# Optimization experiments

Hardware: AMD Instinct MI355X
Metric: run time of the kernel (lower is better)

## Reference

```python
import jax, jax.numpy as jnp
import numpy as np

B, F, T = 4, 2048, 2048
CF, CT = 1024, 1024
H, DH = 16, 64
ALPHA = 1.0 / np.sqrt(DH).astype(np.float32)


def setup_inputs() -> dict:
    key = jax.random.key(0)
    ks = jax.random.split(key, 8)
    s = 0.02  # trunc_normal-ish init scale
    return {
        "from_tensor": jax.random.normal(ks[0], (B, F, CF), jnp.float32),
        "to_tensor": jax.random.normal(ks[1], (B, T, CT), jnp.float32),
        "mask": jax.random.randint(ks[2], (B, F, T), 0, 2, jnp.int32),
        "Wq": jax.random.normal(ks[3], (CF, H * DH), jnp.float32) * s,
        "bq": jnp.zeros((H * DH,), jnp.float32),
        "Wk": jax.random.normal(ks[4], (CT, H * DH), jnp.float32) * s,
        "bk": jnp.zeros((H * DH,), jnp.float32),
        "Wv": jax.random.normal(ks[5], (CT, H * DH), jnp.float32) * s,
        "bv": jnp.zeros((H * DH,), jnp.float32),
    }


def reference(from_tensor, to_tensor, mask, Wq, bq, Wk, bk, Wv, bv):
    # projections (nn.Linear with no activation)
    q = from_tensor @ Wq + bq          # [B,F,H*DH]
    k = to_tensor @ Wk + bk            # [B,T,H*DH]
    v = to_tensor @ Wv + bv            # [B,T,H*DH]
    q = q.reshape(B, F, H, DH)         # query: [..., F, H, DH]
    k = k.reshape(B, T, DH, H)         # key:   [..., T, DH, H]  (self._shape[::-1])
    v = v.reshape(B, T, H, DH)
    # score = transpose(q,-3,-2) @ transpose(k,-3,-1) * alpha -> [B,H,F,T]
    score = jnp.einsum("bfhd,btdh->bhft", q, k) * ALPHA
    if mask is not None:
        adder = (1.0 - mask[:, None].astype(score.dtype)) * -100000.0  # [B,1,F,T]
        score = score + adder
    probs = jax.nn.softmax(score, axis=-1)  # dropout p=0.0 -> identity
    # context = probs @ transpose(v,-3,-2), then transpose back: [B,F,H,DH]
    context = jnp.einsum("bhft,bthd->bfhd", probs, v)
    return context.reshape(B, F, H * DH)
```

## Files before the change

kernel.cpp:

```cpp
#include <hip/hip_runtime.h>
#include <type_traits>

typedef __bf16 bf16_t;
typedef __attribute__((ext_vector_type(8))) __bf16 bf16x8;
typedef __attribute__((ext_vector_type(4))) float f32x4;
typedef __attribute__((ext_vector_type(16))) float f32x16;

__device__ __forceinline__ void async16(const void* g, void* lds) {
  __builtin_amdgcn_global_load_lds((const __attribute__((address_space(1))) unsigned int*)g,
                                   (__attribute__((address_space(3))) unsigned int*)lds, 16, 0, 0);
}

__device__ __forceinline__ unsigned pk2(float lo, float hi) {
  unsigned short a = __builtin_bit_cast(unsigned short, (__bf16)lo);
  unsigned short b = __builtin_bit_cast(unsigned short, (__bf16)hi);
  return (unsigned)a | ((unsigned)b << 16);
}

__device__ __forceinline__ void plswap(unsigned& a, unsigned& b) {
#if __has_builtin(__builtin_amdgcn_permlane32_swap)
  auto r = __builtin_amdgcn_permlane32_swap((int)a, (int)b, false, false);
  a = (unsigned)r[0];
  b = (unsigned)r[1];
#else
  const bool hb = (threadIdx.x & 32) != 0;
  unsigned bx = (unsigned)__shfl_xor((int)b, 32);
  unsigned ax = (unsigned)__shfl_xor((int)a, 32);
  unsigned na = hb ? bx : a;
  unsigned nb = hb ? b : ax;
  a = na; b = nb;
#endif
}

__global__ __launch_bounds__(256) void prep_kernel(const int* __restrict__ mask, unsigned long long* __restrict__ mb,
                                                   const float* __restrict__ Wq, const float* __restrict__ Wk,
                                                   const float* __restrict__ Wv, bf16_t* __restrict__ Wt,
                                                   const float* __restrict__ from, bf16_t* __restrict__ inbF,
                                                   const float* __restrict__ to_, bf16_t* __restrict__ inbT) {
  const int bid = blockIdx.x, tid = threadIdx.x;
  if (bid < 2048) {
    const int lane = tid & 63, w = tid >> 6;
    for (int i = 0; i < 32; ++i) {
      size_t word = (size_t)bid * 128 + (size_t)i * 4 + w;
      unsigned long long bits = __ballot(mask[word * 64 + lane] != 0);
      if (lane == 0) mb[word] = bits;
    }
  } else if (bid < 3584) {
    const int idx = bid - 2048;
    const int z = idx >> 9, r = idx & 511;
    const float* src = (z == 0) ? Wq : ((z == 1) ? Wk : Wv);
    const float sc = (z == 0) ? 0.18033688011112042f : 1.0f;
    bf16_t* dst = Wt + (size_t)z * 1024 * 1024;
    const int n = (r & 15) * 64 + (tid & 63);
    const int k8 = (r >> 4) * 4 + (tid >> 6);
    bf16x8 o;
#pragma unroll
    for (int j = 0; j < 8; ++j) o[j] = (__bf16)(src[(size_t)(k8 * 8 + j) * 1024 + n] * sc);
    *(bf16x8*)(dst + (size_t)n * 1024 + k8 * 8) = o;
  } else {
    const bool isF = bid < 7680;
    const size_t i = (size_t)(bid - (isF ? 3584 : 7680)) * 256 + tid;
    const float4* in4 = (const float4*)(isF ? from : to_);
    bf16_t* outp = isF ? inbF : inbT;
    float4 a = in4[i * 2], b = in4[i * 2 + 1];
    bf16x8 o;
    o[0] = (__bf16)a.x; o[1] = (__bf16)a.y; o[2] = (__bf16)a.z; o[3] = (__bf16)a.w;
    o[4] = (__bf16)b.x; o[5] = (__bf16)b.y; o[6] = (__bf16)b.z; o[7] = (__bf16)b.w;
    *(bf16x8*)(outp + i * 8) = o;
  }
}

__global__ __launch_bounds__(256) void proj_kernel(const bf16_t* __restrict__ inbF, const bf16_t* __restrict__ inbT,
                                                   const bf16_t* __restrict__ Wt,
                                                   const float* __restrict__ bq, const float* __restrict__ bk,
                                                   const float* __restrict__ bv,
                                                   bf16_t* __restrict__ Qw, bf16_t* __restrict__ Kw,
                                                   bf16_t* __restrict__ Vw) {
  __shared__ __align__(16) unsigned char smem[33792];
  bf16_t* se = (bf16_t*)smem;
  const int z = blockIdx.z;
  const bf16_t* A = (z == 0) ? inbF : inbT;
  const bf16_t* Wz = Wt + (size_t)z * 1024 * 1024;
  const float* bias = (z == 0) ? bq : ((z == 1) ? bk : bv);
  bf16_t* dst = (z == 0) ? Qw : ((z == 1) ? Kw : Vw);
  const float bscale = (z == 0) ? 0.18033688011112042f : 1.0f;

  const int tid = threadIdx.x, lane = tid & 63, w = tid >> 6;
  const int m0 = blockIdx.x * 128, n0 = blockIdx.y * 128;
  const int wm = (w >> 1) * 64, wn = (w & 1) * 64;
  const int r = lane & 15, kq = lane >> 4;
  const int srow = lane >> 2, sslot = lane & 3;
  f32x4 acc[4][4] = {};

  auto stage = [&](int buf, int k0) {
    bf16_t* Ad = se + buf * 4096;
    bf16_t* Bd = se + 8192 + buf * 4096;
#pragma unroll
    for (int it = 0; it < 2; ++it) {
      const int c = it * 4 + w;
      const int row = c * 16 + srow;
      async16(A + (size_t)(m0 + row) * 1024 + k0 + ((sslot ^ (row & 3)) * 8), Ad + c * 512);
      async16(Wz + (size_t)(n0 + row) * 1024 + k0 + ((sslot ^ (row & 3)) * 8), Bd + c * 512);
    }
  };

  stage(0, 0);
  __syncthreads();
  for (int tile = 0; tile < 32; ++tile) {
    const int cur = tile & 1;
    if (tile < 31) stage(cur ^ 1, (tile + 1) * 32);
    const bf16_t* Al = se + cur * 4096;
    const bf16_t* Bl = se + 8192 + cur * 4096;
    bf16x8 af[4], bfr[4];
#pragma unroll
    for (int i = 0; i < 4; ++i) {
      const int ra = wm + i * 16 + r;
      af[i] = *(const bf16x8*)(Al + ra * 32 + ((kq ^ (ra & 3)) * 8));
      const int rb = wn + i * 16 + r;
      bfr[i] = *(const bf16x8*)(Bl + rb * 32 + ((kq ^ (rb & 3)) * 8));
    }
    __builtin_amdgcn_s_setprio(1);
#pragma unroll
    for (int i = 0; i < 4; ++i)
#pragma unroll
      for (int j = 0; j < 4; ++j)
        acc[i][j] = __builtin_amdgcn_mfma_f32_16x16x32_bf16(af[i], bfr[j], acc[i][j], 0, 0, 0);
    __builtin_amdgcn_s_setprio(0);
    __syncthreads();
  }

  bf16_t* Cl = se;
  float bvv[4];
#pragma unroll
  for (int j = 0; j < 4; ++j) bvv[j] = bias[n0 + wn + j * 16 + r] * bscale;
#pragma unroll
  for (int i = 0; i < 4; ++i)
#pragma unroll
    for (int j = 0; j < 4; ++j)
#pragma unroll
      for (int g = 0; g < 4; ++g)
        Cl[(wm + i * 16 + kq * 4 + g) * 132 + wn + j * 16 + r] = (__bf16)(acc[i][j][g] + bvv[j]);
  __syncthreads();

  const int b = m0 >> 11, sbase = m0 & 2047;
  if (z == 0) {
#pragma unroll
    for (int q = 0; q < 8; ++q) {
      const int cid = q * 256 + tid;
      const int m = cid >> 4, c = (cid >> 3) & 1, d8 = cid & 7;
      bf16x8 val = *(const bf16x8*)(Cl + m * 132 + c * 64 + d8 * 8);
      *(bf16x8*)(dst + ((size_t)(b * 16 + (n0 >> 6) + c) * 2048 + sbase + m) * 64 + d8 * 8) = val;
    }
  } else if (z == 1) {
#pragma unroll
    for (int q = 0; q < 8; ++q) {
      const int cid = q * 256 + tid;
      const int hh = cid >> 7, m = cid & 127;
      bf16x8 val;
#pragma unroll
      for (int dd = 0; dd < 8; ++dd) val[dd] = Cl[m * 132 + dd * 16 + hh];
      *(bf16x8*)(dst + ((size_t)(b * 16 + hh) * 2048 + sbase + m) * 64 + (n0 >> 4)) = val;
    }
  } else {
#pragma unroll
    for (int q = 0; q < 8; ++q) {
      const int cid = q * 256 + tid;
      const int nl = cid >> 4, m8 = cid & 15;
      bf16x8 val;
#pragma unroll
      for (int s = 0; s < 8; ++s) val[s] = Cl[(m8 * 8 + s) * 132 + nl];
      const int hh = (n0 >> 6) + (nl >> 6), dd = nl & 63;
      *(bf16x8*)(dst + ((size_t)(b * 16 + hh) * 64 + dd) * 2048 + sbase + m8 * 8) = val;
    }
  }
}

__global__ __launch_bounds__(256, 2) void attn_kernel(const bf16_t* __restrict__ Q, const bf16_t* __restrict__ K,
                                                      const bf16_t* __restrict__ VT,
                                                      const unsigned long long* __restrict__ mb,
                                                      float* __restrict__ out) {
  __shared__ __align__(16) unsigned char smem[65536];
  bf16_t* se = (bf16_t*)smem;
  const int tid = threadIdx.x, lane = tid & 63, w = tid >> 6;
  const int cl = lane & 31, hi = lane >> 5;

  const int lid = blockIdx.x + 8 * (blockIdx.y + 16 * blockIdx.z);
  const int xcd = lid & 7, q_ = lid >> 3;
  const int pairIdx = xcd * 8 + (q_ & 7);
  const int f0 = (q_ >> 3) * 256;
  const int h = pairIdx & 15, b = pairIdx >> 4;

  const size_t bh = (size_t)b * 16 + h;
  const int fw = f0 + w * 64;

  const bf16_t* Qb = Q + (bh * 2048 + fw) * 64;
  bf16x8 qf[2][4];
#pragma unroll
  for (int fb = 0; fb < 2; ++fb)
#pragma unroll
    for (int ks = 0; ks < 4; ++ks)
      qf[fb][ks] = *(const bf16x8*)(Qb + (fb * 32 + cl) * 64 + ks * 16 + hi * 8);

  f32x16 Of[2][2] = {};
  float lacc[2] = {0.f, 0.f};
  bf16x8 paw[2][4];

  const unsigned long long* mrow[2];
  mrow[0] = mb + ((size_t)b * 2048 + fw + cl) * 32;
  mrow[1] = mb + ((size_t)b * 2048 + fw + 32 + cl) * 32;

  const int row8 = lane >> 3, slot = lane & 7;
  const int swz = (slot ^ row8) * 8;
  const bf16_t* kgb[2];
  const bf16_t* vgb[2];
#pragma unroll
  for (int it = 0; it < 2; ++it) {
    const int row = it * 32 + w * 8 + row8;
    kgb[it] = K + (bh * 2048 + row) * 64 + swz;
    vgb[it] = VT + (bh * 64 + row) * 2048 + swz;
  }

  auto stage_k = [&](int buf, int tile) {
    bf16_t* kd = se + buf * 4096 + w * 512;
#pragma unroll
    for (int it = 0; it < 2; ++it)
      async16(kgb[it] + (size_t)tile * 4096, kd + it * 2048);
  };
  auto stage_v = [&](int buf, int tile) {
    bf16_t* vd = se + 16384 + buf * 4096 + w * 512;
#pragma unroll
    for (int it = 0; it < 2; ++it)
      async16(vgb[it] + (size_t)tile * 64, vd + it * 2048);
  };

  auto pv_step = [&](int vs) {
    const bf16_t* Vl = se + 16384 + vs * 4096;
    __builtin_amdgcn_s_setprio(1);
#pragma unroll
    for (int db = 0; db < 2; ++db) {
      const int vrow0 = db * 32 + cl;
#pragma unroll
      for (int kt = 0; kt < 4; ++kt) {
        bf16x8 vf = *(const bf16x8*)(Vl + vrow0 * 64 + (((2 * kt + hi) ^ (vrow0 & 7)) * 8));
        Of[0][db] = __builtin_amdgcn_mfma_f32_32x32x16_bf16(paw[0][kt], vf, Of[0][db], 0, 0, 0);
        Of[1][db] = __builtin_amdgcn_mfma_f32_32x32x16_bf16(paw[1][kt], vf, Of[1][db], 0, 0, 0);
      }
    }
    __builtin_amdgcn_s_setprio(0);
  };

  unsigned long long m[4][2];
  stage_k(0, 0); stage_v(0, 0);
  stage_k(1, 1); stage_v(1, 1);
  m[0][0] = mrow[0][0];
  m[0][1] = mrow[1][0];

  auto body = [&](auto Sc, auto lastc, int tile) {
    constexpr int S = decltype(Sc)::value;
    constexpr bool last = decltype(lastc)::value;
    if constexpr (last) {
      asm volatile("s_waitcnt vmcnt(0)" ::: "memory");
    } else {
      asm volatile("s_waitcnt vmcnt(6)" ::: "memory");
    }
    __builtin_amdgcn_s_barrier();
    __builtin_amdgcn_sched_barrier(0);
    if (tile + 2 < 32) {
      stage_k((S + 2) & 3, tile + 2);
      stage_v((S + 2) & 3, tile + 2);
    }
    if (tile + 1 < 32) {
      m[(S + 1) & 3][0] = mrow[0][tile + 1];
      m[(S + 1) & 3][1] = mrow[1][tile + 1];
    }
    const bf16_t* Kl = se + S * 4096;

    f32x16 st0[2], st1[2];
#pragma unroll
    for (int fb = 0; fb < 2; ++fb) {
      const unsigned nm0 = ~((unsigned)(m[S][fb] >> (4 * hi)));
      const unsigned nm1 = ~((unsigned)(m[S][fb] >> (32 + 4 * hi)));
#pragma unroll
      for (int q = 0; q < 4; ++q)
#pragma unroll
        for (int e = 0; e < 4; ++e) {
          const int idx = q * 4 + e;
          const int pos = e + 8 * q;
          st0[fb][idx] = __uint_as_float(((unsigned)(((int)(nm0 << (31 - pos))) >> 31)) & 0xC6EA6000u);
          st1[fb][idx] = __uint_as_float(((unsigned)(((int)(nm1 << (31 - pos))) >> 31)) & 0xC6EA6000u);
        }
    }

    {
      const int krow = cl;
      __builtin_amdgcn_s_setprio(1);
#pragma unroll
      for (int ks = 0; ks < 4; ++ks) {
        bf16x8 kf = *(const bf16x8*)(Kl + krow * 64 + (((2 * ks + hi) ^ (krow & 7)) * 8));
        st0[0] = __builtin_amdgcn_mfma_f32_32x32x16_bf16(kf, qf[0][ks], st0[0], 0, 0, 0);
        st0[1] = __builtin_amdgcn_mfma_f32_32x32x16_bf16(kf, qf[1][ks], st0[1], 0, 0, 0);
      }
      __builtin_amdgcn_s_setprio(0);
    }

    if (tile > 0) pv_step((S + 3) & 3);

    {
      const int krow = 32 + cl;
      __builtin_amdgcn_s_setprio(1);
#pragma unroll
      for (int ks = 0; ks < 4; ++ks) {
        bf16x8 kf = *(const bf16x8*)(Kl + krow * 64 + (((2 * ks + hi) ^ (krow & 7)) * 8));
        st1[0] = __builtin_amdgcn_mfma_f32_32x32x16_bf16(kf, qf[0][ks], st1[0], 0, 0, 0);
        st1[1] = __builtin_amdgcn_mfma_f32_32x32x16_bf16(kf, qf[1][ks], st1[1], 0, 0, 0);
      }
      __builtin_amdgcn_s_setprio(0);
    }

#pragma unroll
    for (int ts = 0; ts < 2; ++ts) {
#pragma unroll
      for (int fb = 0; fb < 2; ++fb) {
        const f32x16& stf = (ts == 0) ? st0[fb] : st1[fb];
        float pv[16];
#pragma unroll
        for (int q = 0; q < 4; ++q)
#pragma unroll
          for (int e = 0; e < 4; ++e) {
            const int idx = q * 4 + e;
            float p = __builtin_amdgcn_exp2f(stf[idx]);
            lacc[fb] += p;
            pv[idx] = p;
          }
#pragma unroll
        for (int kl = 0; kl < 2; ++kl) {
          const int qa = 2 * kl, qb = qa + 1;
          unsigned x0 = pk2(pv[qa * 4 + 0], pv[qa * 4 + 1]);
          unsigned y0 = pk2(pv[qb * 4 + 0], pv[qb * 4 + 1]);
          unsigned x1 = pk2(pv[qa * 4 + 2], pv[qa * 4 + 3]);
          unsigned y1 = pk2(pv[qb * 4 + 2], pv[qb * 4 + 3]);
          plswap(x0, y0);
          plswap(x1, y1);
          union { unsigned u[4]; bf16x8 v; } tmp;
          tmp.u[0] = x0; tmp.u[1] = x1; tmp.u[2] = y0; tmp.u[3] = y1;
          paw[fb][ts * 2 + kl] = tmp.v;
        }
      }
    }
  };

  using s0 = std::integral_constant<int, 0>;
  using s1 = std::integral_constant<int, 1>;
  using s2 = std::integral_constant<int, 2>;
  using s3 = std::integral_constant<int, 3>;
  using bF = std::integral_constant<bool, false>;
  using bT = std::integral_constant<bool, true>;

  for (int t = 0; t < 28; t += 4) {
    body(s0{}, bF{}, t);
    body(s1{}, bF{}, t + 1);
    body(s2{}, bF{}, t + 2);
    body(s3{}, bF{}, t + 3);
  }
  body(s0{}, bF{}, 28);
  body(s1{}, bF{}, 29);
  body(s2{}, bF{}, 30);
  body(s3{}, bT{}, 31);
  pv_step(3);

#pragma unroll
  for (int fb = 0; fb < 2; ++fb) lacc[fb] += __shfl_xor(lacc[fb], 32);
  float* lsh = (float*)smem;
  if (hi == 0) {
    lsh[w * 64 + cl] = lacc[0];
    lsh[w * 64 + 32 + cl] = lacc[1];
  }
#pragma unroll
  for (int fb = 0; fb < 2; ++fb)
#pragma unroll
    for (int q = 0; q < 4; ++q)
#pragma unroll
      for (int e = 0; e < 4; ++e) {
        const int idx = q * 4 + e;
        const int row = e + 8 * q + 4 * hi;
        const float li = 1.0f / lsh[w * 64 + fb * 32 + row];
        const size_t orow = ((size_t)b * 2048 + fw + fb * 32 + row) * 1024 + h * 64;
        out[orow + cl] = Of[fb][0][idx] * li;
        out[orow + 32 + cl] = Of[fb][1][idx] * li;
      }
}

extern "C" void kernel_launch(void* const* d_in, const int* in_sizes, int n_in,
                              void* d_out, int out_size, void* d_ws, size_t ws_size,
                              hipStream_t stream) {
  (void)in_sizes; (void)n_in; (void)out_size; (void)ws_size;
  const float* from = (const float*)d_in[0];
  const float* to_  = (const float*)d_in[1];
  const int*   mask = (const int*)d_in[2];
  const float* Wq = (const float*)d_in[3];
  const float* bq = (const float*)d_in[4];
  const float* Wk = (const float*)d_in[5];
  const float* bk = (const float*)d_in[6];
  const float* Wv = (const float*)d_in[7];
  const float* bv = (const float*)d_in[8];
  float* out = (float*)d_out;
  char* ws = (char*)d_ws;

  bf16_t* Qw = (bf16_t*)(ws);
  bf16_t* Kw = (bf16_t*)(ws + (size_t)(1u << 24));
  bf16_t* Vw = (bf16_t*)(ws + (size_t)(2u << 24));
  bf16_t* Wt = (bf16_t*)(ws + (size_t)(3u << 24));
  unsigned long long* mbits = (unsigned long long*)(ws + (size_t)(3u << 24) + (size_t)(6u << 20));
  bf16_t* inbF = (bf16_t*)(ws + (size_t)(3u << 24) + (size_t)(8u << 20));
  bf16_t* inbT = (bf16_t*)d_out;

  prep_kernel<<<11776, 256, 0, stream>>>(mask, mbits, Wq, Wk, Wv, Wt, from, inbF, to_, inbT);
  proj_kernel<<<dim3(64, 8, 3), 256, 0, stream>>>(inbF, inbT, Wt, bq, bk, bv, Qw, Kw, Vw);
  attn_kernel<<<dim3(8, 16, 4), 256, 0, stream>>>(Qw, Kw, Vw, mbits, out);
}
```

Measured before the change: 206.6 us.

## Process two KV tiles per barrier and drop MFMA priority hints

Splits the loop body into separate helpers (mask init, QK, PV, softmax) and runs two KV tiles per barrier instead of one. Each pair waits for all outstanding loads with vmcnt(0), then issues prefetches for tiles t+2 and t+3 at different points inside the pair. The aim is to halve barrier and wait overhead. The s_setprio hints are removed, and PV no longer sits between the two QK halves. In exchange the async-copy pipeline becomes shallower and waits are stricter. Refilling the t+3 buffer without a barrier may race with other waves still reading that buffer's V data.

After: 446.3 us. 2.16x slower.

```diff
diff --git a/kernel.cpp b/kernel.cpp
--- a/kernel.cpp
+++ b/kernel.cpp
@@ -204,6 +204,7 @@
   f32x16 Of[2][2] = {};
   float lacc[2] = {0.f, 0.f};
   bf16x8 paw[2][4];
+  f32x16 st0[2], st1[2];
 
   const unsigned long long* mrow[2];
   mrow[0] = mb + ((size_t)b * 2048 + fw + cl) * 32;
@@ -233,53 +234,13 @@
       async16(vgb[it] + (size_t)tile * 64, vd + it * 2048);
   };
 
-  auto pv_step = [&](int vs) {
-    const bf16_t* Vl = se + 16384 + vs * 4096;
-    __builtin_amdgcn_s_setprio(1);
-#pragma unroll
-    for (int db = 0; db < 2; ++db) {
-      const int vrow0 = db * 32 + cl;
-#pragma unroll
-      for (int kt = 0; kt < 4; ++kt) {
-        bf16x8 vf = *(const bf16x8*)(Vl + vrow0 * 64 + (((2 * kt + hi) ^ (vrow0 & 7)) * 8));
-        Of[0][db] = __builtin_amdgcn_mfma_f32_32x32x16_bf16(paw[0][kt], vf, Of[0][db], 0, 0, 0);
-        Of[1][db] = __builtin_amdgcn_mfma_f32_32x32x16_bf16(paw[1][kt], vf, Of[1][db], 0, 0, 0);
-      }
-    }
-    __builtin_amdgcn_s_setprio(0);
-  };
-
   unsigned long long m[4][2];
-  stage_k(0, 0); stage_v(0, 0);
-  stage_k(1, 1); stage_v(1, 1);
-  m[0][0] = mrow[0][0];
-  m[0][1] = mrow[1][0];
-
-  auto body = [&](auto Sc, auto lastc, int tile) {
-    constexpr int S = decltype(Sc)::value;
-    constexpr bool last = decltype(lastc)::value;
-    if constexpr (last) {
-      asm volatile("s_waitcnt vmcnt(0)" ::: "memory");
-    } else {
-      asm volatile("s_waitcnt vmcnt(6)" ::: "memory");
-    }
-    __builtin_amdgcn_s_barrier();
-    __builtin_amdgcn_sched_barrier(0);
-    if (tile + 2 < 32) {
-      stage_k((S + 2) & 3, tile + 2);
-      stage_v((S + 2) & 3, tile + 2);
-    }
-    if (tile + 1 < 32) {
-      m[(S + 1) & 3][0] = mrow[0][tile + 1];
-      m[(S + 1) & 3][1] = mrow[1][tile + 1];
-    }
-    const bf16_t* Kl = se + S * 4096;
-
-    f32x16 st0[2], st1[2];
+
+  auto cinit = [&](int ms) {
 #pragma unroll
     for (int fb = 0; fb < 2; ++fb) {
-      const unsigned nm0 = ~((unsigned)(m[S][fb] >> (4 * hi)));
-      const unsigned nm1 = ~((unsigned)(m[S][fb] >> (32 + 4 * hi)));
+      const unsigned nm0 = ~((unsigned)(m[ms][fb] >> (4 * hi)));
+      const unsigned nm1 = ~((unsigned)(m[ms][fb] >> (32 + 4 * hi)));
 #pragma unroll
       for (int q = 0; q < 4; ++q)
 #pragma unroll
@@ -290,33 +251,44 @@
           st1[fb][idx] = __uint_as_float(((unsigned)(((int)(nm1 << (31 - pos))) >> 31)) & 0xC6EA6000u);
         }
     }
-
+  };
+
+  auto qk = [&](const bf16_t* Kl) {
     {
       const int krow = cl;
-      __builtin_amdgcn_s_setprio(1);
 #pragma unroll
       for (int ks = 0; ks < 4; ++ks) {
         bf16x8 kf = *(const bf16x8*)(Kl + krow * 64 + (((2 * ks + hi) ^ (krow & 7)) * 8));
         st0[0] = __builtin_amdgcn_mfma_f32_32x32x16_bf16(kf, qf[0][ks], st0[0], 0, 0, 0);
         st0[1] = __builtin_amdgcn_mfma_f32_32x32x16_bf16(kf, qf[1][ks], st0[1], 0, 0, 0);
       }
-      __builtin_amdgcn_s_setprio(0);
-    }
-
-    if (tile > 0) pv_step((S + 3) & 3);
-
+    }
     {
       const int krow = 32 + cl;
-      __builtin_amdgcn_s_setprio(1);
 #pragma unroll
       for (int ks = 0; ks < 4; ++ks) {
         bf16x8 kf = *(const bf16x8*)(Kl + krow * 64 + (((2 * ks + hi) ^ (krow & 7)) * 8));
         st1[0] = __builtin_amdgcn_mfma_f32_32x32x16_bf16(kf, qf[0][ks], st1[0], 0, 0, 0);
         st1[1] = __builtin_amdgcn_mfma_f32_32x32x16_bf16(kf, qf[1][ks], st1[1], 0, 0, 0);
       }
-      __builtin_amdgcn_s_setprio(0);
-    }
-
+    }
+  };
+
+  auto pv_step = [&](int vs) {
+    const bf16_t* Vl = se + 16384 + vs * 4096;
+#pragma unroll
+    for (int db = 0; db < 2; ++db) {
+      const int vrow0 = db * 32 + cl;
+#pragma unroll
+      for (int kt = 0; kt < 4; ++kt) {
+        bf16x8 vf = *(const bf16x8*)(Vl + vrow0 * 64 + (((2 * kt + hi) ^ (vrow0 & 7)) * 8));
+        Of[0][db] = __builtin_amdgcn_mfma_f32_32x32x16_bf16(paw[0][kt], vf, Of[0][db], 0, 0, 0);
+        Of[1][db] = __builtin_amdgcn_mfma_f32_32x32x16_bf16(paw[1][kt], vf, Of[1][db], 0, 0, 0);
+      }
+    }
+  };
+
+  auto sm = [&]() {
 #pragma unroll
     for (int ts = 0; ts < 2; ++ts) {
 #pragma unroll
@@ -349,23 +321,42 @@
     }
   };
 
-  using s0 = std::integral_constant<int, 0>;
-  using s1 = std::integral_constant<int, 1>;
-  using s2 = std::integral_constant<int, 2>;
-  using s3 = std::integral_constant<int, 3>;
-  using bF = std::integral_constant<bool, false>;
-  using bT = std::integral_constant<bool, true>;
-
-  for (int t = 0; t < 28; t += 4) {
-    body(s0{}, bF{}, t);
-    body(s1{}, bF{}, t + 1);
-    body(s2{}, bF{}, t + 2);
-    body(s3{}, bF{}, t + 3);
-  }
-  body(s0{}, bF{}, 28);
-  body(s1{}, bF{}, 29);
-  body(s2{}, bF{}, 30);
-  body(s3{}, bT{}, 31);
+  stage_k(0, 0); stage_v(0, 0);
+  stage_k(1, 1); stage_v(1, 1);
+  m[0][0] = mrow[0][0]; m[0][1] = mrow[1][0];
+  m[1][0] = mrow[0][1]; m[1][1] = mrow[1][1];
+
+  auto pairf = [&](auto Sc, int t) {
+    constexpr int S = decltype(Sc)::value;
+    asm volatile("s_waitcnt vmcnt(0)" ::: "memory");
+    __builtin_amdgcn_s_barrier();
+    __builtin_amdgcn_sched_barrier(0);
+    if (t + 2 < 32) {
+      m[(S + 2) & 3][0] = mrow[0][t + 2];
+      m[(S + 2) & 3][1] = mrow[1][t + 2];
+      stage_k((S + 2) & 3, t + 2);
+      stage_v((S + 2) & 3, t + 2);
+    }
+    cinit(S);
+    qk(se + S * 4096);
+    if (t > 0) pv_step((S + 3) & 3);
+    sm();
+    if (t + 3 < 32) {
+      m[(S + 3) & 3][0] = mrow[0][t + 3];
+      m[(S + 3) & 3][1] = mrow[1][t + 3];
+      stage_k((S + 3) & 3, t + 3);
+      stage_v((S + 3) & 3, t + 3);
+    }
+    cinit((S + 1) & 3);
+    qk(se + ((S + 1) & 3) * 4096);
+    pv_step(S);
+    sm();
+  };
+
+  for (int t = 0; t < 32; t += 4) {
+    pairf(std::integral_constant<int, 0>{}, t);
+    pairf(std::integral_constant<int, 2>{}, t + 2);
+  }
   pv_step(3);
 
 #pragma unroll
```
